# Kernel optimization log

Hardware: AMD Instinct MI355X
Metric: run time of the kernel (lower is better)

The kernel has to match this reference:

```python
import jax, jax.numpy as jnp
import numpy as np

B, T, C = 4, 2048, 768
H = 12  # n_head; head_dim = C // H = 64


def setup_inputs() -> dict:
    key = jax.random.key(0)
    k1, k2, k3, k4, k5 = jax.random.split(key, 5)
    scale = 0.02
    return {
        "x": jax.random.normal(k1, (B, T, C), dtype=jnp.float32),
        "w_attn": jax.random.normal(k2, (C, 3 * C), dtype=jnp.float32) * scale,
        "b_attn": jax.random.normal(k3, (3 * C,), dtype=jnp.float32) * scale,
        "w_proj": jax.random.normal(k4, (C, C), dtype=jnp.float32) * scale,
        "b_proj": jax.random.normal(k5, (C,), dtype=jnp.float32) * scale,
    }


def reference(x, w_attn, b_attn, w_proj, b_proj):
    Bx, Tx, Cx = x.shape
    hd = Cx // H  # head dim
    qkv = x @ w_attn + b_attn                       # [B, T, 3C]
    q, k, v = jnp.split(qkv, 3, axis=2)
    # [B, T, H, hd] -> [B, H, T, hd]
    q = q.reshape(Bx, Tx, H, hd).transpose(0, 2, 1, 3)
    k = k.reshape(Bx, Tx, H, hd).transpose(0, 2, 1, 3)
    v = v.reshape(Bx, Tx, H, hd).transpose(0, 2, 1, 3)
    att = jnp.einsum('bhqd,bhkd->bhqk', q, k) / jnp.sqrt(jnp.float32(hd))
    causal = jnp.tril(jnp.ones((Tx, Tx), dtype=bool))
    att = jnp.where(causal[None, None, :, :], att, -jnp.inf)
    att = jax.nn.softmax(att, axis=-1)
    y = jnp.einsum('bhqk,bhkd->bhqd', att, v)       # [B, H, T, hd]
    y = y.transpose(0, 2, 1, 3).reshape(Bx, Tx, Cx)
    return y @ w_proj + b_proj
```

## Files before the change

kernel.cpp:

```cpp
#include <hip/hip_runtime.h>
#include <hip/hip_bf16.h>

using f32x4 = __attribute__((ext_vector_type(4))) float;
using s16x8 = __attribute__((ext_vector_type(8))) short;

#define MFMA16x16x32(a, b, c) __builtin_amdgcn_mfma_f32_16x16x32_bf16((a), (b), (c), 0, 0, 0)

#define AS_G(p) ((const __attribute__((address_space(1))) void*)(p))
#define AS_L(p) ((__attribute__((address_space(3))) void*)(p))

#define BARRIER_LGKM() do { \
    asm volatile("s_waitcnt lgkmcnt(0)" ::: "memory"); \
    __builtin_amdgcn_s_barrier(); \
} while (0)

static __device__ __forceinline__ unsigned short f2bf(float f) {
    unsigned int u = __float_as_uint(f);
    u = (u + 0x7fffu + ((u >> 16) & 1u)) >> 16;
    return (unsigned short)u;
}
static __device__ __forceinline__ unsigned int cvt_pk_bf2(float lo, float hi) {
    unsigned int r;
    asm("v_cvt_pk_bf16_f32 %0, %1, %2" : "=v"(r) : "v"(lo), "v"(hi));
    return r;
}
static __device__ __forceinline__ int swz128(int r, int c) { return (r * 128 + c) ^ ((r & 7) << 4); }

__global__ void cvt_f32_bf16(const float* __restrict__ in, unsigned short* __restrict__ out, int n) {
    int i = (blockIdx.x * blockDim.x + threadIdx.x) * 4;
    int stride = gridDim.x * blockDim.x * 4;
    for (; i < n; i += stride) {
        float4 v = *(const float4*)(in + i);
        ushort4 o;
        o.x = f2bf(v.x); o.y = f2bf(v.y); o.z = f2bf(v.z); o.w = f2bf(v.w);
        *(ushort4*)(out + i) = o;
    }
}

__global__ __launch_bounds__(256)
void transpose_cvt_tiled(const float* __restrict__ w, unsigned short* __restrict__ wt,
                         int K, int N) {
    __shared__ float tile[32][33];
    const int tid = threadIdx.x;
    const int tx = tid & 31, ty = tid >> 5;
    const int n0 = blockIdx.x * 32, k0 = blockIdx.y * 32;
#pragma unroll
    for (int r = 0; r < 4; r++)
        tile[ty * 4 + r][tx] = w[(size_t)(k0 + ty * 4 + r) * N + n0 + tx];
    __syncthreads();
#pragma unroll
    for (int r = 0; r < 4; r++)
        wt[(size_t)(n0 + ty * 4 + r) * K + k0 + tx] = f2bf(tile[tx][ty * 4 + r]);
}

template <bool OUT_BF16>
__global__ __launch_bounds__(256, 2)
void gemm_bt(const unsigned short* __restrict__ A, const unsigned short* __restrict__ Bt,
             const float* __restrict__ bias, void* __restrict__ Cout,
             unsigned short* __restrict__ Vt,
             int M, int N, int K, int ldc, int qcols, float qscale) {
    __shared__ char smem[65536];
    const int tid = threadIdx.x, wid = tid >> 6, lane = tid & 63;
    const int g = lane >> 4, lr = lane & 15;
    const int m0 = blockIdx.y * 128, n0 = blockIdx.x * 128;
    const int wm = wid >> 1, wn = wid & 1;

    f32x4 acc[4][4];
#pragma unroll
    for (int i = 0; i < 4; i++)
#pragma unroll
        for (int j = 0; j < 4; j++) acc[i][j] = f32x4{0.f, 0.f, 0.f, 0.f};

    const int rbase = lane >> 3;
    const int cSw = ((lane & 7) << 4) ^ (rbase << 4);

    auto STAGE = [&](int buf, int kt) {
        char* base = smem + buf * 32768;
#pragma unroll
        for (int ww = 0; ww < 4; ww++) {
            int w = wid * 4 + ww;
            int r = w * 8 + rbase;
            const unsigned short* srcA = A + (size_t)(m0 + r) * K + kt + (cSw >> 1);
            __builtin_amdgcn_global_load_lds(AS_G(srcA), AS_L(base + w * 1024), 16, 0, 0);
            const unsigned short* srcB = Bt + (size_t)(n0 + r) * K + kt + (cSw >> 1);
            __builtin_amdgcn_global_load_lds(AS_G(srcB), AS_L(base + 16384 + w * 1024), 16, 0, 0);
        }
    };

    const int nk = K >> 6;
    STAGE(0, 0);

    for (int t = 0; t < nk; t++) {
        if (t + 1 < nk) {
            STAGE((t + 1) & 1, (t + 1) << 6);
            asm volatile("s_waitcnt vmcnt(8)" ::: "memory");
        } else {
            asm volatile("s_waitcnt vmcnt(0)" ::: "memory");
        }
        __builtin_amdgcn_s_barrier();
        char* cbase = smem + (t & 1) * 32768;
#pragma unroll
        for (int ks = 0; ks < 2; ks++) {
            s16x8 af[4], bfr[4];
#pragma unroll
            for (int i = 0; i < 4; i++)
                af[i] = *(const s16x8*)(cbase + swz128(wm * 64 + i * 16 + lr, ks * 64 + g * 16));
#pragma unroll
            for (int j = 0; j < 4; j++)
                bfr[j] = *(const s16x8*)(cbase + 16384 + swz128(wn * 64 + j * 16 + lr, ks * 64 + g * 16));
#pragma unroll
            for (int i = 0; i < 4; i++)
#pragma unroll
                for (int j = 0; j < 4; j++)
                    acc[i][j] = MFMA16x16x32(af[i], bfr[j], acc[i][j]);
        }
        BARRIER_LGKM();
    }

#pragma unroll
    for (int j = 0; j < 4; j++) {
        int c = n0 + wn * 64 + j * 16 + lr;
        float bv = bias[c];
        float cscale = (c < qcols) ? qscale : 1.0f;
        if (Vt != nullptr && c >= 1536) {
            int h = (c - 1536) >> 6, d = (c - 1536) & 63;
#pragma unroll
            for (int i = 0; i < 4; i++) {
                int r0 = m0 + wm * 64 + i * 16 + g * 4;
                int bb = r0 >> 11, t0 = r0 & 2047;
                ushort4 o4;
                o4.x = f2bf(acc[i][j][0] + bv);
                o4.y = f2bf(acc[i][j][1] + bv);
                o4.z = f2bf(acc[i][j][2] + bv);
                o4.w = f2bf(acc[i][j][3] + bv);
                *(ushort4*)(Vt + ((((size_t)bb * 12 + h) * 64 + d) << 11) + t0) = o4;
            }
        } else {
#pragma unroll
            for (int i = 0; i < 4; i++) {
#pragma unroll
                for (int rg = 0; rg < 4; rg++) {
                    int r = m0 + wm * 64 + i * 16 + g * 4 + rg;
                    float val = (acc[i][j][rg] + bv) * cscale;
                    if constexpr (OUT_BF16)
                        ((unsigned short*)Cout)[(size_t)r * ldc + c] = f2bf(val);
                    else
                        ((float*)Cout)[(size_t)r * ldc + c] = val;
                }
            }
        }
    }
}

__global__ __launch_bounds__(256, 2)
void attn_kernel(const unsigned short* __restrict__ qk, const unsigned short* __restrict__ Vt,
                 unsigned short* __restrict__ y) {
    __shared__ char smem[40960];
    const int tid = threadIdx.x, wid = tid >> 6, lane = tid & 63;
    const int g = lane >> 4, lr = lane & 15;
    const int T = 2048;

    const int s = blockIdx.x;
    const int xcd = s & 7, i = s >> 3;
    const int grp = xcd * 6 + (i >> 4);
    const int qpi = i & 15;
    const int h = grp % 12, b = grp / 12;

    const int krow = tid >> 2;
    const int kcol = (tid & 3) * 32;

    for (int pp = 0; pp < 2; pp++) {
        const int qt = pp ? (31 - qpi) : qpi;
        const int q0 = qt * 64;

        const unsigned short* qrow = qk + (size_t)(b * T + q0 + wid * 16 + lr) * 1536 + h * 64;
        s16x8 aq[2];
        aq[0] = *(const s16x8*)(qrow + g * 8);
        aq[1] = *(const s16x8*)(qrow + 32 + g * 8);

        float l_acc = 0.f;
        f32x4 o[4];
#pragma unroll
        for (int r = 0; r < 4; r++) o[r] = f32x4{0.f, 0.f, 0.f, 0.f};

        const unsigned short* pkBase = qk + (size_t)(b * T + krow) * 1536 + 768 + h * 64 + (kcol >> 1);
        const unsigned short* pvBase = Vt + ((((size_t)b * 12 + h) * 64 + krow) << 11) + (kcol >> 1);

        const int nt = qt + 1;

        s16x8 k0 = *(const s16x8*)(pkBase);
        s16x8 k1 = *(const s16x8*)(pkBase + 8);
        s16x8 v0 = *(const s16x8*)(pvBase);
        s16x8 v1 = *(const s16x8*)(pvBase + 8);
        *(s16x8*)(smem + swz128(krow, kcol)) = k0;
        *(s16x8*)(smem + swz128(krow, kcol + 16)) = k1;
        *(s16x8*)(smem + 16384 + swz128(krow, kcol)) = v0;
        *(s16x8*)(smem + 16384 + swz128(krow, kcol + 16)) = v1;
        if (nt > 1) {
            const unsigned short* pk = pkBase + (size_t)64 * 1536;
            k0 = *(const s16x8*)(pk);
            k1 = *(const s16x8*)(pk + 8);
            const unsigned short* pv = pvBase + 64;
            v0 = *(const s16x8*)(pv);
            v1 = *(const s16x8*)(pv + 8);
        }
        BARRIER_LGKM();

        for (int t = 0; t < nt; t++) {
            char* kbase = smem + (t & 1) * 8192;
            char* vbase = smem + 16384 + (t & 1) * 8192;

            f32x4 st[4];
            __builtin_amdgcn_s_setprio(1);
#pragma unroll
            for (int nf = 0; nf < 4; nf++) {
                f32x4 sf = f32x4{0.f, 0.f, 0.f, 0.f};
#pragma unroll
                for (int ks = 0; ks < 2; ks++) {
                    int jj = nf * 16 + lr;
                    s16x8 ak = *(const s16x8*)(kbase + swz128(jj, (ks * 32 + g * 8) * 2));
                    sf = MFMA16x16x32(ak, aq[ks], sf);
                }
                st[nf] = sf;
            }
            __builtin_amdgcn_s_setprio(0);

            const bool diag = (t == nt - 1);
            const int q_rel = wid * 16 + lr;
#pragma unroll
            for (int nf = 0; nf < 4; nf++) {
#pragma unroll
                for (int rg = 0; rg < 4; rg++) {
                    float p = exp2f(st[nf][rg]);
                    if (diag && (nf * 16 + g * 4 + rg > q_rel)) p = 0.f;
                    st[nf][rg] = p;
                    l_acc += p;
                }
            }

            char* pbase = smem + 32768 + wid * 2048;
#pragma unroll
            for (int nf = 0; nf < 4; nf++) {
                uint2 dw;
                dw.x = cvt_pk_bf2(st[nf][0], st[nf][1]);
                dw.y = cvt_pk_bf2(st[nf][2], st[nf][3]);
                *(uint2*)(pbase + swz128(lr, nf * 32 + g * 8)) = dw;
            }
            s16x8 pf[2];
#pragma unroll
            for (int ks = 0; ks < 2; ks++)
                pf[ks] = *(const s16x8*)(pbase + swz128(lr, ks * 64 + g * 16));

            __builtin_amdgcn_s_setprio(1);
#pragma unroll
            for (int nf = 0; nf < 4; nf++) {
#pragma unroll
                for (int ks = 0; ks < 2; ks++) {
                    int d = nf * 16 + lr;
                    s16x8 bv = *(const s16x8*)(vbase + swz128(d, ks * 64 + g * 16));
                    o[nf] = MFMA16x16x32(pf[ks], bv, o[nf]);
                }
            }
            __builtin_amdgcn_s_setprio(0);

            if (t + 1 < nt) {
                char* kn = smem + ((t + 1) & 1) * 8192;
                char* vn = smem + 16384 + ((t + 1) & 1) * 8192;
                *(s16x8*)(kn + swz128(krow, kcol)) = k0;
                *(s16x8*)(kn + swz128(krow, kcol + 16)) = k1;
                *(s16x8*)(vn + swz128(krow, kcol)) = v0;
                *(s16x8*)(vn + swz128(krow, kcol + 16)) = v1;
                if (t + 2 < nt) {
                    const unsigned short* pk = pkBase + (size_t)(t + 2) * 64 * 1536;
                    k0 = *(const s16x8*)(pk);
                    k1 = *(const s16x8*)(pk + 8);
                    const unsigned short* pv = pvBase + (t + 2) * 64;
                    v0 = *(const s16x8*)(pv);
                    v1 = *(const s16x8*)(pv + 8);
                }
            }
            BARRIER_LGKM();
        }

        float l = l_acc;
        l += __shfl_xor(l, 16, 64);
        l += __shfl_xor(l, 32, 64);
        float linv = 1.0f / l;
        float linv_q[4];
#pragma unroll
        for (int rg = 0; rg < 4; rg++)
            linv_q[rg] = __shfl(linv, (lane & 48) | (g * 4 + rg), 64);
#pragma unroll
        for (int nf = 0; nf < 4; nf++) {
#pragma unroll
            for (int rg = 0; rg < 4; rg++) {
                int row = b * T + q0 + wid * 16 + g * 4 + rg;
                int col = h * 64 + nf * 16 + lr;
                y[(size_t)row * 768 + col] = f2bf(o[nf][rg] * linv_q[rg]);
            }
        }
    }
}

extern "C" void kernel_launch(void* const* d_in, const int* in_sizes, int n_in,
                              void* d_out, int out_size, void* d_ws, size_t ws_size,
                              hipStream_t stream) {
    const float* x      = (const float*)d_in[0];
    const float* w_attn = (const float*)d_in[1];
    const float* b_attn = (const float*)d_in[2];
    const float* w_proj = (const float*)d_in[3];
    const float* b_proj = (const float*)d_in[4];

    char* ws = (char*)d_ws;
    unsigned short* qk  = (unsigned short*)(ws);
    unsigned short* Vt  = (unsigned short*)(ws + 25165824);
    unsigned short* wTa = (unsigned short*)(ws + 37748736);
    unsigned short* wTp = (unsigned short*)(ws + 41287680);

    const bool big = ws_size >= (size_t)55050240;
    unsigned short* xb = (unsigned short*)d_out;
    unsigned short* yb = big ? (unsigned short*)(ws + 42467328)
                             : (unsigned short*)((char*)d_out + 12582912);
    float* projOut = big ? (float*)d_out : (float*)ws;

    cvt_f32_bf16<<<2048, 256, 0, stream>>>(x, xb, 8192 * 768);
    transpose_cvt_tiled<<<dim3(72, 24), 256, 0, stream>>>(w_attn, wTa, 768, 2304);
    transpose_cvt_tiled<<<dim3(24, 24), 256, 0, stream>>>(w_proj, wTp, 768, 768);

    gemm_bt<true><<<dim3(18, 64), 256, 0, stream>>>(xb, wTa, b_attn, (void*)qk, Vt,
                                                    8192, 2304, 768, 1536, 768, 0.1803368801111244f);
    attn_kernel<<<768, 256, 0, stream>>>(qk, Vt, yb);
    gemm_bt<false><<<dim3(6, 64), 256, 0, stream>>>(yb, wTp, b_proj, (void*)projOut, nullptr,
                                                    8192, 768, 768, 768, 0, 1.0f);
    if (!big)
        hipMemcpyAsync(d_out, projOut, 25165824, hipMemcpyDeviceToDevice, stream);
}
```

Measured before the change: 134.3 us.

## Share K/V tiles across paired query tiles and fuse prologue conversion kernels

The attention kernel now processes both paired query tiles (qpi and 31-qpi) in one pass over the K/V stream. Each loaded K/V tile is reused by both query tiles, so the short tile's key range is no longer loaded a second time. Separately, the x conversion and both weight transpose-conversions are merged into one prologue launch to cut launch overhead. The cost is more live registers (two sets of accumulators and Q fragments), which may hurt occupancy under the 2-block launch bound.

```diff
diff --git a/kernel.cpp b/kernel.cpp
--- a/kernel.cpp
+++ b/kernel.cpp
@@ -26,31 +26,41 @@
 }
 static __device__ __forceinline__ int swz128(int r, int c) { return (r * 128 + c) ^ ((r & 7) << 4); }
 
-__global__ void cvt_f32_bf16(const float* __restrict__ in, unsigned short* __restrict__ out, int n) {
-    int i = (blockIdx.x * blockDim.x + threadIdx.x) * 4;
-    int stride = gridDim.x * blockDim.x * 4;
-    for (; i < n; i += stride) {
-        float4 v = *(const float4*)(in + i);
-        ushort4 o;
-        o.x = f2bf(v.x); o.y = f2bf(v.y); o.z = f2bf(v.z); o.w = f2bf(v.w);
-        *(ushort4*)(out + i) = o;
-    }
-}
-
 __global__ __launch_bounds__(256)
-void transpose_cvt_tiled(const float* __restrict__ w, unsigned short* __restrict__ wt,
-                         int K, int N) {
+void prologue_kernel(const float* __restrict__ x, unsigned short* __restrict__ xb,
+                     const float* __restrict__ w_attn, unsigned short* __restrict__ wTa,
+                     const float* __restrict__ w_proj, unsigned short* __restrict__ wTp) {
     __shared__ float tile[32][33];
-    const int tid = threadIdx.x;
-    const int tx = tid & 31, ty = tid >> 5;
-    const int n0 = blockIdx.x * 32, k0 = blockIdx.y * 32;
-#pragma unroll
-    for (int r = 0; r < 4; r++)
-        tile[ty * 4 + r][tx] = w[(size_t)(k0 + ty * 4 + r) * N + n0 + tx];
-    __syncthreads();
-#pragma unroll
-    for (int r = 0; r < 4; r++)
-        wt[(size_t)(n0 + ty * 4 + r) * K + k0 + tx] = f2bf(tile[tx][ty * 4 + r]);
+    const int bid = blockIdx.x, tid = threadIdx.x;
+    if (bid < 2048) {
+        const int n = 8192 * 768;
+        int i = (bid * 256 + tid) * 4;
+        const int stride = 2048 * 256 * 4;
+        for (; i < n; i += stride) {
+            float4 v = *(const float4*)(x + i);
+            ushort4 o;
+            o.x = f2bf(v.x); o.y = f2bf(v.y); o.z = f2bf(v.z); o.w = f2bf(v.w);
+            *(ushort4*)(xb + i) = o;
+        }
+    } else {
+        const float* w; unsigned short* wt; int K, N, bx, by;
+        if (bid < 3776) {
+            int id = bid - 2048; w = w_attn; wt = wTa; K = 768; N = 2304;
+            bx = id % 72; by = id / 72;
+        } else {
+            int id = bid - 3776; w = w_proj; wt = wTp; K = 768; N = 768;
+            bx = id % 24; by = id / 24;
+        }
+        const int tx = tid & 31, ty = tid >> 5;
+        const int n0 = bx * 32, k0 = by * 32;
+#pragma unroll
+        for (int r = 0; r < 4; r++)
+            tile[ty * 4 + r][tx] = w[(size_t)(k0 + ty * 4 + r) * N + n0 + tx];
+        __syncthreads();
+#pragma unroll
+        for (int r = 0; r < 4; r++)
+            wt[(size_t)(n0 + ty * 4 + r) * K + k0 + tx] = f2bf(tile[tx][ty * 4 + r]);
+    }
 }
 
 template <bool OUT_BF16>
@@ -165,51 +175,56 @@
     const int grp = xcd * 6 + (i >> 4);
     const int qpi = i & 15;
     const int h = grp % 12, b = grp / 12;
+    const int qtA = qpi, qtB = 31 - qpi;
+    const int q0A = qtA * 64, q0B = qtB * 64;
 
     const int krow = tid >> 2;
     const int kcol = (tid & 3) * 32;
 
-    for (int pp = 0; pp < 2; pp++) {
-        const int qt = pp ? (31 - qpi) : qpi;
-        const int q0 = qt * 64;
-
-        const unsigned short* qrow = qk + (size_t)(b * T + q0 + wid * 16 + lr) * 1536 + h * 64;
-        s16x8 aq[2];
-        aq[0] = *(const s16x8*)(qrow + g * 8);
-        aq[1] = *(const s16x8*)(qrow + 32 + g * 8);
-
-        float l_acc = 0.f;
-        f32x4 o[4];
-#pragma unroll
-        for (int r = 0; r < 4; r++) o[r] = f32x4{0.f, 0.f, 0.f, 0.f};
-
-        const unsigned short* pkBase = qk + (size_t)(b * T + krow) * 1536 + 768 + h * 64 + (kcol >> 1);
-        const unsigned short* pvBase = Vt + ((((size_t)b * 12 + h) * 64 + krow) << 11) + (kcol >> 1);
-
-        const int nt = qt + 1;
-
-        s16x8 k0 = *(const s16x8*)(pkBase);
-        s16x8 k1 = *(const s16x8*)(pkBase + 8);
-        s16x8 v0 = *(const s16x8*)(pvBase);
-        s16x8 v1 = *(const s16x8*)(pvBase + 8);
-        *(s16x8*)(smem + swz128(krow, kcol)) = k0;
-        *(s16x8*)(smem + swz128(krow, kcol + 16)) = k1;
-        *(s16x8*)(smem + 16384 + swz128(krow, kcol)) = v0;
-        *(s16x8*)(smem + 16384 + swz128(krow, kcol + 16)) = v1;
-        if (nt > 1) {
-            const unsigned short* pk = pkBase + (size_t)64 * 1536;
-            k0 = *(const s16x8*)(pk);
-            k1 = *(const s16x8*)(pk + 8);
-            const unsigned short* pv = pvBase + 64;
-            v0 = *(const s16x8*)(pv);
-            v1 = *(const s16x8*)(pv + 8);
-        }
-        BARRIER_LGKM();
-
-        for (int t = 0; t < nt; t++) {
-            char* kbase = smem + (t & 1) * 8192;
-            char* vbase = smem + 16384 + (t & 1) * 8192;
-
+    const unsigned short* qrowA = qk + (size_t)(b * T + q0A + wid * 16 + lr) * 1536 + h * 64;
+    const unsigned short* qrowB = qk + (size_t)(b * T + q0B + wid * 16 + lr) * 1536 + h * 64;
+    s16x8 aqA[2], aqB[2];
+    aqA[0] = *(const s16x8*)(qrowA + g * 8);
+    aqA[1] = *(const s16x8*)(qrowA + 32 + g * 8);
+    aqB[0] = *(const s16x8*)(qrowB + g * 8);
+    aqB[1] = *(const s16x8*)(qrowB + 32 + g * 8);
+
+    float lA = 0.f, lB = 0.f;
+    f32x4 oA[4], oB[4];
+#pragma unroll
+    for (int r = 0; r < 4; r++) { oA[r] = f32x4{0.f, 0.f, 0.f, 0.f}; oB[r] = f32x4{0.f, 0.f, 0.f, 0.f}; }
+
+    const unsigned short* pkBase = qk + (size_t)(b * T + krow) * 1536 + 768 + h * 64 + (kcol >> 1);
+    const unsigned short* pvBase = Vt + ((((size_t)b * 12 + h) * 64 + krow) << 11) + (kcol >> 1);
+
+    const int ntA = qtA + 1, ntB = qtB + 1;
+
+    s16x8 k0 = *(const s16x8*)(pkBase);
+    s16x8 k1 = *(const s16x8*)(pkBase + 8);
+    s16x8 v0 = *(const s16x8*)(pvBase);
+    s16x8 v1 = *(const s16x8*)(pvBase + 8);
+    *(s16x8*)(smem + swz128(krow, kcol)) = k0;
+    *(s16x8*)(smem + swz128(krow, kcol + 16)) = k1;
+    *(s16x8*)(smem + 16384 + swz128(krow, kcol)) = v0;
+    *(s16x8*)(smem + 16384 + swz128(krow, kcol + 16)) = v1;
+    if (ntB > 1) {
+        const unsigned short* pk = pkBase + (size_t)64 * 1536;
+        k0 = *(const s16x8*)(pk);
+        k1 = *(const s16x8*)(pk + 8);
+        const unsigned short* pv = pvBase + 64;
+        v0 = *(const s16x8*)(pv);
+        v1 = *(const s16x8*)(pv + 8);
+    }
+    BARRIER_LGKM();
+
+    char* const pbase = smem + 32768 + wid * 2048;
+    const int q_rel = wid * 16 + lr;
+
+    for (int t = 0; t < ntB; t++) {
+        char* kbase = smem + (t & 1) * 8192;
+        char* vbase = smem + 16384 + (t & 1) * 8192;
+
+        {
             f32x4 st[4];
             __builtin_amdgcn_s_setprio(1);
 #pragma unroll
@@ -217,28 +232,24 @@
                 f32x4 sf = f32x4{0.f, 0.f, 0.f, 0.f};
 #pragma unroll
                 for (int ks = 0; ks < 2; ks++) {
-                    int jj = nf * 16 + lr;
-                    s16x8 ak = *(const s16x8*)(kbase + swz128(jj, (ks * 32 + g * 8) * 2));
-                    sf = MFMA16x16x32(ak, aq[ks], sf);
+                    s16x8 ak = *(const s16x8*)(kbase + swz128(nf * 16 + lr, (ks * 32 + g * 8) * 2));
+                    sf = MFMA16x16x32(ak, aqB[ks], sf);
                 }
                 st[nf] = sf;
             }
             __builtin_amdgcn_s_setprio(0);
 
-            const bool diag = (t == nt - 1);
-            const int q_rel = wid * 16 + lr;
-#pragma unroll
-            for (int nf = 0; nf < 4; nf++) {
+            const bool diag = (t == ntB - 1);
+#pragma unroll
+            for (int nf = 0; nf < 4; nf++)
 #pragma unroll
                 for (int rg = 0; rg < 4; rg++) {
                     float p = exp2f(st[nf][rg]);
                     if (diag && (nf * 16 + g * 4 + rg > q_rel)) p = 0.f;
                     st[nf][rg] = p;
-                    l_acc += p;
-                }
-            }
-
-            char* pbase = smem + 32768 + wid * 2048;
+                    lB += p;
+                }
+
 #pragma unroll
             for (int nf = 0; nf < 4; nf++) {
                 uint2 dw;
@@ -256,33 +267,85 @@
             for (int nf = 0; nf < 4; nf++) {
 #pragma unroll
                 for (int ks = 0; ks < 2; ks++) {
-                    int d = nf * 16 + lr;
-                    s16x8 bv = *(const s16x8*)(vbase + swz128(d, ks * 64 + g * 16));
-                    o[nf] = MFMA16x16x32(pf[ks], bv, o[nf]);
+                    s16x8 bv = *(const s16x8*)(vbase + swz128(nf * 16 + lr, ks * 64 + g * 16));
+                    oB[nf] = MFMA16x16x32(pf[ks], bv, oB[nf]);
                 }
             }
             __builtin_amdgcn_s_setprio(0);
-
-            if (t + 1 < nt) {
-                char* kn = smem + ((t + 1) & 1) * 8192;
-                char* vn = smem + 16384 + ((t + 1) & 1) * 8192;
-                *(s16x8*)(kn + swz128(krow, kcol)) = k0;
-                *(s16x8*)(kn + swz128(krow, kcol + 16)) = k1;
-                *(s16x8*)(vn + swz128(krow, kcol)) = v0;
-                *(s16x8*)(vn + swz128(krow, kcol + 16)) = v1;
-                if (t + 2 < nt) {
-                    const unsigned short* pk = pkBase + (size_t)(t + 2) * 64 * 1536;
-                    k0 = *(const s16x8*)(pk);
-                    k1 = *(const s16x8*)(pk + 8);
-                    const unsigned short* pv = pvBase + (t + 2) * 64;
-                    v0 = *(const s16x8*)(pv);
-                    v1 = *(const s16x8*)(pv + 8);
-                }
-            }
-            BARRIER_LGKM();
-        }
-
-        float l = l_acc;
+        }
+
+        if (t < ntA) {
+            f32x4 st[4];
+            __builtin_amdgcn_s_setprio(1);
+#pragma unroll
+            for (int nf = 0; nf < 4; nf++) {
+                f32x4 sf = f32x4{0.f, 0.f, 0.f, 0.f};
+#pragma unroll
+                for (int ks = 0; ks < 2; ks++) {
+                    s16x8 ak = *(const s16x8*)(kbase + swz128(nf * 16 + lr, (ks * 32 + g * 8) * 2));
+                    sf = MFMA16x16x32(ak, aqA[ks], sf);
+                }
+                st[nf] = sf;
+            }
+            __builtin_amdgcn_s_setprio(0);
+
+            const bool diag = (t == ntA - 1);
+#pragma unroll
+            for (int nf = 0; nf < 4; nf++)
+#pragma unroll
+                for (int rg = 0; rg < 4; rg++) {
+                    float p = exp2f(st[nf][rg]);
+                    if (diag && (nf * 16 + g * 4 + rg > q_rel)) p = 0.f;
+                    st[nf][rg] = p;
+                    lA += p;
+                }
+
+#pragma unroll
+            for (int nf = 0; nf < 4; nf++) {
+                uint2 dw;
+                dw.x = cvt_pk_bf2(st[nf][0], st[nf][1]);
+                dw.y = cvt_pk_bf2(st[nf][2], st[nf][3]);
+                *(uint2*)(pbase + swz128(lr, nf * 32 + g * 8)) = dw;
+            }
+            s16x8 pf[2];
+#pragma unroll
+            for (int ks = 0; ks < 2; ks++)
+                pf[ks] = *(const s16x8*)(pbase + swz128(lr, ks * 64 + g * 16));
+
+            __builtin_amdgcn_s_setprio(1);
+#pragma unroll
+            for (int nf = 0; nf < 4; nf++) {
+#pragma unroll
+                for (int ks = 0; ks < 2; ks++) {
+                    s16x8 bv = *(const s16x8*)(vbase + swz128(nf * 16 + lr, ks * 64 + g * 16));
+                    oA[nf] = MFMA16x16x32(pf[ks], bv, oA[nf]);
+                }
+            }
+            __builtin_amdgcn_s_setprio(0);
+        }
+
+        if (t + 1 < ntB) {
+            char* kn = smem + ((t + 1) & 1) * 8192;
+            char* vn = smem + 16384 + ((t + 1) & 1) * 8192;
+            *(s16x8*)(kn + swz128(krow, kcol)) = k0;
+            *(s16x8*)(kn + swz128(krow, kcol + 16)) = k1;
+            *(s16x8*)(vn + swz128(krow, kcol)) = v0;
+            *(s16x8*)(vn + swz128(krow, kcol + 16)) = v1;
+            if (t + 2 < ntB) {
+                const unsigned short* pk = pkBase + (size_t)(t + 2) * 64 * 1536;
+                k0 = *(const s16x8*)(pk);
+                k1 = *(const s16x8*)(pk + 8);
+                const unsigned short* pv = pvBase + (t + 2) * 64;
+                v0 = *(const s16x8*)(pv);
+                v1 = *(const s16x8*)(pv + 8);
+            }
+        }
+        BARRIER_LGKM();
+    }
+
+#pragma unroll
+    for (int which = 0; which < 2; which++) {
+        float l = which ? lB : lA;
         l += __shfl_xor(l, 16, 64);
         l += __shfl_xor(l, 32, 64);
         float linv = 1.0f / l;
@@ -290,6 +353,8 @@
 #pragma unroll
         for (int rg = 0; rg < 4; rg++)
             linv_q[rg] = __shfl(linv, (lane & 48) | (g * 4 + rg), 64);
+        const int q0 = which ? q0B : q0A;
+        f32x4* o = which ? oB : oA;
 #pragma unroll
         for (int nf = 0; nf < 4; nf++) {
 #pragma unroll
@@ -323,9 +388,7 @@
                              : (unsigned short*)((char*)d_out + 12582912);
     float* projOut = big ? (float*)d_out : (float*)ws;
 
-    cvt_f32_bf16<<<2048, 256, 0, stream>>>(x, xb, 8192 * 768);
-    transpose_cvt_tiled<<<dim3(72, 24), 256, 0, stream>>>(w_attn, wTa, 768, 2304);
-    transpose_cvt_tiled<<<dim3(24, 24), 256, 0, stream>>>(w_proj, wTp, 768, 768);
+    prologue_kernel<<<4352, 256, 0, stream>>>(x, xb, w_attn, wTa, w_proj, wTp);
 
     gemm_bt<true><<<dim3(18, 64), 256, 0, stream>>>(xb, wTa, b_attn, (void*)qk, Vt,
                                                     8192, 2304, 768, 1536, 768, 0.1803368801111244f);
```

New measurement: 132.2 us. About the same (-1.6%).
